# Kernel tuning notes

Hardware: AMD Instinct MI355X
Metric: run time of the kernel (lower is better)

The kernel has to match this reference:

```python
import jax, jax.numpy as jnp
import numpy as np

HEADS = 16
PHI = (1.0 + np.sqrt(5.0)) / 2.0


def setup_inputs() -> dict:
    key = jax.random.key(0)
    k1, k2, k3, k4 = jax.random.split(key, 4)
    B, L, D = 2, 2048, 1024
    x = jax.random.normal(k1, (B, L, D), dtype=jnp.float32)
    # nn.Linear(dim, 3*dim, bias=False): store as [D, 3D] for x @ W
    w_qkv = jax.random.normal(k2, (D, 3 * D), dtype=jnp.float32) * (D ** -0.5)
    w_proj = jax.random.normal(k3, (D, D), dtype=jnp.float32) * (D ** -0.5)
    b_proj = jax.random.normal(k4, (D,), dtype=jnp.float32) * 0.01
    return {"x": x, "w_qkv": w_qkv, "w_proj": w_proj, "b_proj": b_proj}


def phi_bias(L):
    # pos[i] = (i * phi) mod 1 ; bias = log(exp(-|pos_i - pos_j|) + 1e-8)
    pos = (jnp.arange(L, dtype=jnp.float32) * PHI) % 1.0
    dist = jnp.abs(pos[:, None] - pos[None, :])  # [L, L]
    return jnp.log(jnp.exp(-dist) + 1e-8)


def reference(x, w_qkv, w_proj, b_proj):
    B, L, D = x.shape
    H = HEADS
    Dh = D // H
    scale = Dh ** -0.5
    qkv = (x @ w_qkv).reshape(B, L, 3, H, Dh)
    q = jnp.transpose(qkv[:, :, 0], (0, 2, 1, 3))  # [B, H, L, Dh]
    k = jnp.transpose(qkv[:, :, 1], (0, 2, 1, 3))
    v = jnp.transpose(qkv[:, :, 2], (0, 2, 1, 3))
    attn = jnp.einsum("bhid,bhjd->bhij", q, k) * scale  # [B, H, L, L]
    attn = attn + phi_bias(L)[None, None]  # additive phi-distance bias
    attn = jax.nn.softmax(attn, axis=-1)
    out = jnp.einsum("bhij,bhjd->bhid", attn, v)  # [B, H, L, Dh]
    out = jnp.transpose(out, (0, 2, 1, 3)).reshape(B, L, D)
    return out @ w_proj + b_proj
```

## Files before the change

kernel.cpp:

```cpp
#include <hip/hip_runtime.h>
#include <math.h>


typedef _Float16 f16;
typedef _Float16 f16x4 __attribute__((ext_vector_type(4)));
typedef _Float16 f16x8 __attribute__((ext_vector_type(8)));
typedef float f32x4 __attribute__((ext_vector_type(4)));

#define MFMA32(a, b, c) __builtin_amdgcn_mfma_f32_16x16x32_f16(a, b, c, 0, 0, 0)

static constexpr int Bsz = 2, Lseq = 2048, Dm = 1024, H = 16, Dh = 64;
static constexpr int Mtot = Bsz * Lseq;
static constexpr int NQKV = 3 * Dm;
static constexpr float PHI_F = 1.61803398874989484820f;
static constexpr float LOG2E = 1.44269504088896f;
static constexpr float QS = 0.125f * LOG2E;
static constexpr float CSTEP = 0.55417527999932633f;

__device__ __forceinline__ void load16_to_lds(const f16* g, f16* l) {
  __builtin_amdgcn_global_load_lds(
      (const __attribute__((address_space(1))) unsigned int*)g,
      (__attribute__((address_space(3))) unsigned int*)l, 16, 0, 0);
}

__global__ __launch_bounds__(256) void prep_fused(
    const float* __restrict__ x, f16* __restrict__ xb,
    const float* __restrict__ wqkv, f16* __restrict__ wqkvT,
    const float* __restrict__ wproj, f16* __restrict__ wpT) {
  __shared__ float tile[32][33];
  int blk = blockIdx.x;
  if (blk < 4096) {
    int i = (blk * 256 + threadIdx.x) * 4;
    float4 v = *reinterpret_cast<const float4*>(x + i);
    f16 t[4] = {(f16)v.x, (f16)v.y, (f16)v.z, (f16)v.w};
    *reinterpret_cast<uint2*>(xb + i) = *reinterpret_cast<uint2*>(t);
    return;
  }
  const float* in;
  f16* out;
  int N, bx, by;
  if (blk < 7168) {
    int local = blk - 4096;
    bx = local % 96; by = local / 96; N = NQKV;
    in = wqkv; out = wqkvT;
  } else {
    int local = blk - 7168;
    bx = local & 31; by = local >> 5; N = Dm;
    in = wproj; out = wpT;
  }
  int n0 = bx * 32, k0 = by * 32;
  int tx = threadIdx.x & 31, ty = threadIdx.x >> 5;
#pragma unroll
  for (int r = 0; r < 32; r += 8)
    tile[ty + r][tx] = in[(size_t)(k0 + ty + r) * N + n0 + tx];
  __syncthreads();
#pragma unroll
  for (int r = 0; r < 32; r += 8)
    out[(size_t)(n0 + ty + r) * Dm + k0 + tx] = (f16)tile[tx][ty + r];
}

template <int MODE>
__global__ __launch_bounds__(256) void gemm_f16(
    const f16* __restrict__ A, const f16* __restrict__ Bt,
    int M, int N, int K,
    f16* __restrict__ qb, f16* __restrict__ kb, f16* __restrict__ vb,
    float* __restrict__ out, const float* __restrict__ bias) {
  constexpr int BM = (MODE == 0) ? 128 : 64;
  constexpr int MI = BM / 32;
  constexpr int AI = BM / 32;
  __shared__ f16 As[BM * 64];
  __shared__ f16 Bs[128 * 64];

  int tid = threadIdx.x;
  int wave = tid >> 6, lane = tid & 63;
  int quad = lane >> 4, l16 = lane & 15;
  int wm = (wave >> 1) * (MI * 16), wn = (wave & 1) * 64;

  int lid = blockIdx.x;
  int xcd = lid & 7, t = lid >> 3;
  int m0, n0;
  if (MODE == 0) {
    int mg = xcd >> 1, ng = xcd & 1;
    m0 = (mg * 8 + t / 12) * 128;
    n0 = (ng * 12 + t % 12) * 128;
  } else {
    m0 = (xcd * 8 + (t >> 3)) * 64;
    n0 = (t & 7) * 128;
  }

  const int gu = (lane & 7) ^ (lane >> 3);
  const f16* gA[AI];
  f16* lA[AI];
#pragma unroll
  for (int i = 0; i < AI; i++) {
    int it = wave * AI + i;
    gA[i] = A + (size_t)(m0 + it * 8 + (lane >> 3)) * K + gu * 8;
    lA[i] = As + it * 512;
  }
  const f16* gB[4];
  f16* lB[4];
#pragma unroll
  for (int i = 0; i < 4; i++) {
    int it = wave * 4 + i;
    gB[i] = Bt + (size_t)(n0 + it * 8 + (lane >> 3)) * K + gu * 8;
    lB[i] = Bs + it * 512;
  }

  f32x4 acc[MI][4] = {};

  for (int k0 = 0; k0 < K; k0 += 64) {
#pragma unroll
    for (int i = 0; i < AI; i++) load16_to_lds(gA[i] + k0, lA[i]);
#pragma unroll
    for (int i = 0; i < 4; i++) load16_to_lds(gB[i] + k0, lB[i]);
    __syncthreads();
#pragma unroll
    for (int s = 0; s < 2; s++) {
      f16x8 a[MI], b[4];
#pragma unroll
      for (int i = 0; i < MI; i++) {
        int row = wm + i * 16 + l16;
        a[i] = *reinterpret_cast<const f16x8*>(
            As + row * 64 + (((s * 4 + quad) ^ (l16 & 7)) * 8));
      }
#pragma unroll
      for (int j = 0; j < 4; j++) {
        int row = wn + j * 16 + l16;
        b[j] = *reinterpret_cast<const f16x8*>(
            Bs + row * 64 + (((s * 4 + quad) ^ (l16 & 7)) * 8));
      }
#pragma unroll
      for (int i = 0; i < MI; i++)
#pragma unroll
        for (int j = 0; j < 4; j++)
          acc[i][j] = MFMA32(a[i], b[j], acc[i][j]);
    }
    __syncthreads();
  }

#pragma unroll
  for (int i = 0; i < MI; i++) {
#pragma unroll
    for (int j = 0; j < 4; j++) {
      int n = n0 + wn + j * 16 + l16;
      if (MODE == 0) {
        int ty = n >> 10;
        int df = n & 1023;
        int h = df >> 6, dh = df & 63;
        int mb = m0 + wm + i * 16 + quad * 4;
        int b = mb >> 11, l = mb & 2047;
        int bhh = b * H + h;
        if (ty == 2) {
          int jj = l & 63;
          int jh = jj >> 5, rem = jj & 31;
          int qd = (rem & 15) >> 2;
          int e0 = (rem >= 16) ? 4 : 0;
          f16x4 tmp;
#pragma unroll
          for (int r = 0; r < 4; r++) tmp[r] = (f16)acc[i][j][r];
          *reinterpret_cast<uint2*>(
              vb + (size_t)bhh * (Dh * Lseq) + (l >> 6) * 4096 + dh * 64 +
              (jh * 4 + qd) * 8 + e0) = *reinterpret_cast<uint2*>(&tmp);
        } else {
          size_t idx = (((size_t)bhh) * Lseq + l) * Dh + dh;
          if (ty == 0) {
#pragma unroll
            for (int r = 0; r < 4; r++)
              qb[idx + (size_t)r * Dh] = (f16)(acc[i][j][r] * QS);
          } else {
#pragma unroll
            for (int r = 0; r < 4; r++)
              kb[idx + (size_t)r * Dh] = (f16)acc[i][j][r];
          }
        }
      } else {
#pragma unroll
        for (int r = 0; r < 4; r++) {
          int m = m0 + wm + i * 16 + quad * 4 + r;
          out[(size_t)m * N + n] = acc[i][j][r] + bias[n];
        }
      }
    }
  }
}

__global__ __launch_bounds__(512, 4) void attn_kernel(
    const f16* __restrict__ qb,
    const f16* __restrict__ kb,
    const f16* __restrict__ vb,
    f16* __restrict__ ctx) {
  __shared__ __align__(16) unsigned char smem[33280];
  f16* Ks = (f16*)smem;
  f16* Vs = (f16*)(smem + 8192);

  int id = blockIdx.x;
  int bh = (id & 7) * 4 + ((id >> 3) >> 4);
  int q0 = ((id >> 3) & 15) * 128;

  int tid = threadIdx.x, wave = tid >> 6, lane = tid & 63;
  int quad = lane >> 4, l16 = lane & 15;
  int jhalf = wave >> 2, qq = wave & 3;

  f16x8 qfrag[2][2];
  float pq[2];
#pragma unroll
  for (int set = 0; set < 2; set++) {
    int q = q0 + qq * 32 + set * 16 + l16;
    const f16* Qrow = qb + ((size_t)bh * Lseq + q) * Dh;
    qfrag[set][0] = *reinterpret_cast<const f16x8*>(Qrow + quad * 8);
    qfrag[set][1] = *reinterpret_cast<const f16x8*>(Qrow + 32 + quad * 8);
    pq[set] = fmodf((float)q * PHI_F, 1.0f);
  }

  float pk[2][4];
#pragma unroll
  for (int jb = 0; jb < 2; jb++)
#pragma unroll
    for (int r = 0; r < 4; r++) {
      int j = jhalf * 32 + jb * 16 + quad * 4 + r;
      pk[jb][r] = fmodf((float)j * PHI_F, 1.0f);
    }

  const f16* Kbh = kb + (size_t)bh * Lseq * Dh;
  const f16* Vbh = vb + (size_t)bh * Dh * Lseq;
  const int gu = (lane & 7) ^ (lane >> 3);
  int g8 = wave * 8 + (lane >> 3);
  const f16* gK = Kbh + (size_t)g8 * Dh + gu * 8;
  const f16* gV = Vbh + (size_t)g8 * 64 + gu * 8;
  f16* lK = Ks + wave * 512;
  f16* lV = Vs + wave * 512;

  const f16 one = (f16)1.0f;
  const f16x8 ones8 = {one, one, one, one, one, one, one, one};

  f32x4 acc_o[2][4] = {};
  f32x4 acc_l[2] = {};

  for (int j0 = 0; j0 < Lseq; j0 += 64) {
    __syncthreads();
    load16_to_lds(gK + (size_t)j0 * Dh, lK);
    load16_to_lds(gV + (size_t)j0 * 64, lV);
    __syncthreads();

    f32x4 accs[2][2] = {};
#pragma unroll
    for (int s = 0; s < 2; s++)
#pragma unroll
      for (int jb = 0; jb < 2; jb++) {
        f16x8 kf = *reinterpret_cast<const f16x8*>(
            Ks + (jhalf * 32 + jb * 16 + l16) * 64 + (((s * 4 + quad) ^ (l16 & 7)) * 8));
        accs[0][jb] = MFMA32(kf, qfrag[0][s], accs[0][jb]);
        accs[1][jb] = MFMA32(kf, qfrag[1][s], accs[1][jb]);
      }

    f16x8 pf8[2];
#pragma unroll
    for (int set = 0; set < 2; set++) {
#pragma unroll
      for (int jb = 0; jb < 2; jb++) {
        float p[4];
#pragma unroll
        for (int r = 0; r < 4; r++) {
          float d = pq[set] - pk[jb][r];
          float arg = fmaf(-LOG2E, fabsf(d), accs[set][jb][r]);
          p[r] = __builtin_amdgcn_exp2f(arg);
        }
        auto lo = __builtin_amdgcn_cvt_pkrtz(p[0], p[1]);
        auto hi = __builtin_amdgcn_cvt_pkrtz(p[2], p[3]);
        pf8[set][jb * 4 + 0] = lo[0];
        pf8[set][jb * 4 + 1] = lo[1];
        pf8[set][jb * 4 + 2] = hi[0];
        pf8[set][jb * 4 + 3] = hi[1];
      }
      acc_l[set] = MFMA32(ones8, pf8[set], acc_l[set]);
    }
#pragma unroll
    for (int jb = 0; jb < 2; jb++)
#pragma unroll
      for (int r = 0; r < 4; r++)
        pk[jb][r] = __builtin_amdgcn_fractf(pk[jb][r] + CSTEP);

#pragma unroll
    for (int dblk = 0; dblk < 4; dblk++) {
      int row = dblk * 16 + l16;
      f16x8 va = *reinterpret_cast<const f16x8*>(
          Vs + row * 64 + (((jhalf * 4 + quad) ^ (l16 & 7)) * 8));
      acc_o[0][dblk] = MFMA32(va, pf8[0], acc_o[0][dblk]);
      acc_o[1][dblk] = MFMA32(va, pf8[1], acc_o[1][dblk]);
    }
  }

  __syncthreads();
  float* Oex = (float*)smem;
  float* Lex = (float*)(smem + 32768);
  if (jhalf == 1) {
#pragma unroll
    for (int set = 0; set < 2; set++) {
#pragma unroll
      for (int dblk = 0; dblk < 4; dblk++)
#pragma unroll
        for (int r = 0; r < 4; r++)
          Oex[(((qq * 2 + set) * 4 + dblk) * 16 + quad * 4 + r) * 16 + l16] =
              acc_o[set][dblk][r];
      if (quad == 0) Lex[(qq * 2 + set) * 16 + l16] = acc_l[set][0];
    }
  }
  __syncthreads();
  if (jhalf == 0) {
    int b = bh >> 4, h = bh & 15;
#pragma unroll
    for (int set = 0; set < 2; set++) {
      float ltot = acc_l[set][0] + Lex[(qq * 2 + set) * 16 + l16];
      float inv = 1.0f / ltot;
      int q = q0 + qq * 32 + set * 16 + l16;
      f16* crow = ctx + (size_t)(b * Lseq + q) * Dm + h * 64;
#pragma unroll
      for (int dblk = 0; dblk < 4; dblk++) {
        f16x4 o;
#pragma unroll
        for (int r = 0; r < 4; r++) {
          float full = acc_o[set][dblk][r] +
              Oex[(((qq * 2 + set) * 4 + dblk) * 16 + quad * 4 + r) * 16 + l16];
          o[r] = (f16)(full * inv);
        }
        *reinterpret_cast<uint2*>(crow + dblk * 16 + quad * 4) =
            *reinterpret_cast<uint2*>(&o);
      }
    }
  }
}

extern "C" void kernel_launch(void* const* d_in, const int* in_sizes, int n_in,
                              void* d_out, int out_size, void* d_ws, size_t ws_size,
                              hipStream_t stream) {
  const float* x      = (const float*)d_in[0];
  const float* w_qkv  = (const float*)d_in[1];
  const float* w_proj = (const float*)d_in[2];
  const float* b_proj = (const float*)d_in[3];
  float* out = (float*)d_out;

  f16* xb    = (f16*)d_ws;
  f16* wqkvT = xb + (size_t)Mtot * Dm;
  f16* wpT   = wqkvT + (size_t)NQKV * Dm;
  f16* qb    = wpT + (size_t)Dm * Dm;
  f16* kb    = qb + (size_t)Bsz * H * Lseq * Dh;
  f16* vb    = kb + (size_t)Bsz * H * Lseq * Dh;
  f16* ctx   = vb + (size_t)Bsz * H * Lseq * Dh;

  prep_fused<<<8192, 256, 0, stream>>>(x, xb, w_qkv, wqkvT, w_proj, wpT);

  gemm_f16<0><<<768, 256, 0, stream>>>(
      xb, wqkvT, Mtot, NQKV, Dm, qb, kb, vb, nullptr, nullptr);

  attn_kernel<<<512, 512, 0, stream>>>(qb, kb, vb, ctx);

  gemm_f16<1><<<512, 256, 0, stream>>>(
      ctx, wpT, Mtot, Dm, Dm, nullptr, nullptr, nullptr, out, b_proj);
}
```

Measured before the change: 180.8 us.

## Double-buffer GEMM LDS tiles with prefetch and enlarge block tiles

```diff
diff --git a/kernel.cpp b/kernel.cpp
--- a/kernel.cpp
+++ b/kernel.cpp
@@ -60,83 +60,99 @@
 }
 
 template <int MODE>
-__global__ __launch_bounds__(256) void gemm_f16(
+__global__ __launch_bounds__(MODE == 0 ? 512 : 256, 2) void gemm_f16(
     const f16* __restrict__ A, const f16* __restrict__ Bt,
     int M, int N, int K,
     f16* __restrict__ qb, f16* __restrict__ kb, f16* __restrict__ vb,
     float* __restrict__ out, const float* __restrict__ bias) {
-  constexpr int BM = (MODE == 0) ? 128 : 64;
-  constexpr int MI = BM / 32;
-  constexpr int AI = BM / 32;
-  __shared__ f16 As[BM * 64];
-  __shared__ f16 Bs[128 * 64];
+  constexpr int BM = (MODE == 0) ? 256 : 128;
+  constexpr int BN = (MODE == 0) ? 256 : 128;
+  constexpr int NW = (MODE == 0) ? 8 : 4;
+  constexpr int MI = (MODE == 0) ? 8 : 4;
+  constexpr int WN = (MODE == 0) ? 4 : 2;
+  __shared__ f16 As[2 * BM * 64];
+  __shared__ f16 Bs[2 * BN * 64];
 
   int tid = threadIdx.x;
   int wave = tid >> 6, lane = tid & 63;
   int quad = lane >> 4, l16 = lane & 15;
-  int wm = (wave >> 1) * (MI * 16), wn = (wave & 1) * 64;
+  int warp_m = wave / WN, warp_n = wave % WN;
+  int wm = warp_m * (MI * 16), wn = warp_n * 64;
 
   int lid = blockIdx.x;
   int xcd = lid & 7, t = lid >> 3;
   int m0, n0;
   if (MODE == 0) {
     int mg = xcd >> 1, ng = xcd & 1;
-    m0 = (mg * 8 + t / 12) * 128;
-    n0 = (ng * 12 + t % 12) * 128;
+    m0 = (mg * 4 + t / 6) * 256;
+    n0 = (ng * 6 + t % 6) * 256;
   } else {
-    m0 = (xcd * 8 + (t >> 3)) * 64;
+    m0 = (xcd * 4 + (t >> 3)) * 128;
     n0 = (t & 7) * 128;
   }
 
   const int gu = (lane & 7) ^ (lane >> 3);
-  const f16* gA[AI];
-  f16* lA[AI];
-#pragma unroll
-  for (int i = 0; i < AI; i++) {
-    int it = wave * AI + i;
-    gA[i] = A + (size_t)(m0 + it * 8 + (lane >> 3)) * K + gu * 8;
-    lA[i] = As + it * 512;
-  }
+  const f16* gA[4];
   const f16* gB[4];
-  f16* lB[4];
 #pragma unroll
   for (int i = 0; i < 4; i++) {
-    int it = wave * 4 + i;
-    gB[i] = Bt + (size_t)(n0 + it * 8 + (lane >> 3)) * K + gu * 8;
-    lB[i] = Bs + it * 512;
-  }
+    int row = (i * NW + wave) * 8 + (lane >> 3);
+    gA[i] = A + (size_t)(m0 + row) * K + gu * 8;
+    gB[i] = Bt + (size_t)(n0 + row) * K + gu * 8;
+  }
+
+  auto stage = [&](int buf, int kn) __attribute__((always_inline)) {
+#pragma unroll
+    for (int i = 0; i < 4; i++)
+      load16_to_lds(gA[i] + kn, As + buf * (BM * 64) + (i * NW + wave) * 512);
+#pragma unroll
+    for (int i = 0; i < 4; i++)
+      load16_to_lds(gB[i] + kn, Bs + buf * (BN * 64) + (i * NW + wave) * 512);
+  };
 
   f32x4 acc[MI][4] = {};
 
-  for (int k0 = 0; k0 < K; k0 += 64) {
-#pragma unroll
-    for (int i = 0; i < AI; i++) load16_to_lds(gA[i] + k0, lA[i]);
-#pragma unroll
-    for (int i = 0; i < 4; i++) load16_to_lds(gB[i] + k0, lB[i]);
-    __syncthreads();
-#pragma unroll
-    for (int s = 0; s < 2; s++) {
-      f16x8 a[MI], b[4];
-#pragma unroll
-      for (int i = 0; i < MI; i++) {
-        int row = wm + i * 16 + l16;
-        a[i] = *reinterpret_cast<const f16x8*>(
-            As + row * 64 + (((s * 4 + quad) ^ (l16 & 7)) * 8));
-      }
-#pragma unroll
-      for (int j = 0; j < 4; j++) {
-        int row = wn + j * 16 + l16;
-        b[j] = *reinterpret_cast<const f16x8*>(
-            Bs + row * 64 + (((s * 4 + quad) ^ (l16 & 7)) * 8));
-      }
-#pragma unroll
-      for (int i = 0; i < MI; i++)
-#pragma unroll
-        for (int j = 0; j < 4; j++)
-          acc[i][j] = MFMA32(a[i], b[j], acc[i][j]);
-    }
-    __syncthreads();
-  }
+  stage(0, 0);
+  stage(1, 64);
+
+  int nt = K >> 6;
+#pragma unroll 1
+  for (int kt = 0; kt < nt; kt++) {
+    int buf = kt & 1;
+    asm volatile("s_waitcnt vmcnt(8)" ::: "memory");
+    __builtin_amdgcn_sched_barrier(0);
+    __builtin_amdgcn_s_barrier();
+    __builtin_amdgcn_sched_barrier(0);
+
+    const f16* Ab = As + buf * (BM * 64) + (wm + l16) * 64;
+    const f16* Bb = Bs + buf * (BN * 64) + (wn + l16) * 64;
+    f16x8 b[4][2];
+#pragma unroll
+    for (int nj = 0; nj < 4; nj++)
+#pragma unroll
+      for (int s = 0; s < 2; s++)
+        b[nj][s] = *reinterpret_cast<const f16x8*>(
+            Bb + nj * 16 * 64 + (((s * 4 + quad) ^ (l16 & 7)) * 8));
+#pragma unroll
+    for (int mi = 0; mi < MI; mi++) {
+      f16x8 a0 = *reinterpret_cast<const f16x8*>(
+          Ab + mi * 16 * 64 + ((quad ^ (l16 & 7)) * 8));
+      f16x8 a1 = *reinterpret_cast<const f16x8*>(
+          Ab + mi * 16 * 64 + (((4 + quad) ^ (l16 & 7)) * 8));
+#pragma unroll
+      for (int nj = 0; nj < 4; nj++) {
+        acc[mi][nj] = MFMA32(a0, b[nj][0], acc[mi][nj]);
+        acc[mi][nj] = MFMA32(a1, b[nj][1], acc[mi][nj]);
+      }
+    }
+
+    __builtin_amdgcn_sched_barrier(0);
+    __builtin_amdgcn_s_barrier();
+    __builtin_amdgcn_sched_barrier(0);
+    int kn = (kt + 2 < nt) ? (kt + 2) * 64 : 0;
+    stage(buf, kn);
+  }
+  asm volatile("s_waitcnt vmcnt(0)" ::: "memory");
 
 #pragma unroll
   for (int i = 0; i < MI; i++) {
@@ -349,11 +365,11 @@
 
   prep_fused<<<8192, 256, 0, stream>>>(x, xb, w_qkv, wqkvT, w_proj, wpT);
 
-  gemm_f16<0><<<768, 256, 0, stream>>>(
+  gemm_f16<0><<<192, 512, 0, stream>>>(
       xb, wqkvT, Mtot, NQKV, Dm, qb, kb, vb, nullptr, nullptr);
 
   attn_kernel<<<512, 512, 0, stream>>>(qb, kb, vb, ctx);
 
-  gemm_f16<1><<<512, 256, 0, stream>>>(
+  gemm_f16<1><<<256, 256, 0, stream>>>(
       ctx, wpT, Mtot, Dm, Dm, nullptr, nullptr, nullptr, out, b_proj);
 }
```

New measurement: 187.4 us. +3.6%, slower.

## Rewrite QKV GEMM as 256x256 tiles with double-buffered LDS pipelining

Applied to the files above, without the earlier changes.

```diff
diff --git a/kernel.cpp b/kernel.cpp
--- a/kernel.cpp
+++ b/kernel.cpp
@@ -21,6 +21,12 @@
   __builtin_amdgcn_global_load_lds(
       (const __attribute__((address_space(1))) unsigned int*)g,
       (__attribute__((address_space(3))) unsigned int*)l, 16, 0, 0);
+}
+
+__device__ __forceinline__ void barrier_fenced() {
+  __builtin_amdgcn_sched_barrier(0);
+  __builtin_amdgcn_s_barrier();
+  __builtin_amdgcn_sched_barrier(0);
 }
 
 __global__ __launch_bounds__(256) void prep_fused(
@@ -59,15 +65,194 @@
     out[(size_t)(n0 + ty + r) * Dm + k0 + tx] = (f16)tile[tx][ty + r];
 }
 
-template <int MODE>
-__global__ __launch_bounds__(256) void gemm_f16(
+__global__ __launch_bounds__(512, 2) void gemm_qkv(
     const f16* __restrict__ A, const f16* __restrict__ Bt,
-    int M, int N, int K,
-    f16* __restrict__ qb, f16* __restrict__ kb, f16* __restrict__ vb,
+    f16* __restrict__ qb, f16* __restrict__ kb, f16* __restrict__ vb) {
+  __shared__ f16 As[2 * 256 * 64];
+  __shared__ f16 Bs[2 * 256 * 64];
+
+  int tid = threadIdx.x;
+  int wave = tid >> 6, lane = tid & 63;
+  int quad = lane >> 4, l16 = lane & 15;
+  int warp_m = wave >> 2, warp_n = wave & 3;
+  int wm = warp_m * 128, wn = warp_n * 64;
+
+  int lid = blockIdx.x;
+  int xcd = lid & 7, t = lid >> 3;
+  int mg = xcd >> 1, ng = xcd & 1;
+  int m0 = (mg * 4 + t / 6) * 256;
+  int n0 = (ng * 6 + t % 6) * 256;
+
+  const int gu = (lane & 7) ^ (lane >> 3);
+  const f16* gAb = A + (size_t)(m0 + wave * 8 + (lane >> 3)) * Dm + gu * 8;
+  const f16* gBb = Bt + (size_t)(n0 + wave * 8 + (lane >> 3)) * Dm + gu * 8;
+
+  auto stageA = [&](int buf, int h, int kn) __attribute__((always_inline)) {
+#pragma unroll
+    for (int i = 0; i < 2; i++)
+      load16_to_lds(gAb + (size_t)(h * 128 + i * 64) * Dm + kn,
+                    As + buf * 16384 + (h * 128 + i * 64 + wave * 8) * 64);
+  };
+  auto stageB = [&](int buf, int h, int kn) __attribute__((always_inline)) {
+#pragma unroll
+    for (int i = 0; i < 2; i++)
+      load16_to_lds(gBb + (size_t)(h * 128 + i * 64) * Dm + kn,
+                    Bs + buf * 16384 + (h * 128 + i * 64 + wave * 8) * 64);
+  };
+
+  f32x4 acc[8][4] = {};
+
+  auto do_tile = [&](int buf, int t_) __attribute__((always_inline)) {
+    const f16* Ab = As + buf * 16384 + (wm + l16) * 64;
+    const f16* Bb = Bs + buf * 16384 + (wn + l16) * 64;
+    int nbuf = buf ^ 1;
+    int kA = ((t_ + 1) & 15) * 64;
+    int kB = ((t_ + 2) & 15) * 64;
+
+    f16x8 a[4][2], b0[2][2], b1[2][2];
+
+#pragma unroll
+    for (int m = 0; m < 4; m++)
+#pragma unroll
+      for (int s = 0; s < 2; s++)
+        a[m][s] = *reinterpret_cast<const f16x8*>(
+            Ab + m * 16 * 64 + (((s * 4 + quad) ^ (l16 & 7)) * 8));
+#pragma unroll
+    for (int n = 0; n < 2; n++)
+#pragma unroll
+      for (int s = 0; s < 2; s++)
+        b0[n][s] = *reinterpret_cast<const f16x8*>(
+            Bb + n * 16 * 64 + (((s * 4 + quad) ^ (l16 & 7)) * 8));
+    stageA(nbuf, 0, kA);
+    barrier_fenced();
+    asm volatile("s_waitcnt lgkmcnt(0)" ::: "memory");
+    __builtin_amdgcn_sched_barrier(0);
+    __builtin_amdgcn_s_setprio(1);
+#pragma unroll
+    for (int m = 0; m < 4; m++)
+#pragma unroll
+      for (int n = 0; n < 2; n++) {
+        acc[m][n] = MFMA32(a[m][0], b0[n][0], acc[m][n]);
+        acc[m][n] = MFMA32(a[m][1], b0[n][1], acc[m][n]);
+      }
+    __builtin_amdgcn_s_setprio(0);
+    barrier_fenced();
+
+#pragma unroll
+    for (int n = 0; n < 2; n++)
+#pragma unroll
+      for (int s = 0; s < 2; s++)
+        b1[n][s] = *reinterpret_cast<const f16x8*>(
+            Bb + (2 + n) * 16 * 64 + (((s * 4 + quad) ^ (l16 & 7)) * 8));
+    stageA(nbuf, 1, kA);
+    barrier_fenced();
+    asm volatile("s_waitcnt lgkmcnt(0)" ::: "memory");
+    __builtin_amdgcn_sched_barrier(0);
+    __builtin_amdgcn_s_setprio(1);
+#pragma unroll
+    for (int m = 0; m < 4; m++)
+#pragma unroll
+      for (int n = 0; n < 2; n++) {
+        acc[m][2 + n] = MFMA32(a[m][0], b1[n][0], acc[m][2 + n]);
+        acc[m][2 + n] = MFMA32(a[m][1], b1[n][1], acc[m][2 + n]);
+      }
+    __builtin_amdgcn_s_setprio(0);
+    barrier_fenced();
+
+#pragma unroll
+    for (int m = 0; m < 4; m++)
+#pragma unroll
+      for (int s = 0; s < 2; s++)
+        a[m][s] = *reinterpret_cast<const f16x8*>(
+            Ab + (4 + m) * 16 * 64 + (((s * 4 + quad) ^ (l16 & 7)) * 8));
+    stageB(buf, 0, kB);
+    barrier_fenced();
+    asm volatile("s_waitcnt lgkmcnt(0)" ::: "memory");
+    __builtin_amdgcn_sched_barrier(0);
+    __builtin_amdgcn_s_setprio(1);
+#pragma unroll
+    for (int m = 0; m < 4; m++)
+#pragma unroll
+      for (int n = 0; n < 2; n++) {
+        acc[4 + m][n] = MFMA32(a[m][0], b0[n][0], acc[4 + m][n]);
+        acc[4 + m][n] = MFMA32(a[m][1], b0[n][1], acc[4 + m][n]);
+      }
+    __builtin_amdgcn_s_setprio(0);
+    barrier_fenced();
+
+    stageB(buf, 1, kB);
+    asm volatile("s_waitcnt vmcnt(4)" ::: "memory");
+    barrier_fenced();
+    __builtin_amdgcn_s_setprio(1);
+#pragma unroll
+    for (int m = 0; m < 4; m++)
+#pragma unroll
+      for (int n = 0; n < 2; n++) {
+        acc[4 + m][2 + n] = MFMA32(a[m][0], b1[n][0], acc[4 + m][2 + n]);
+        acc[4 + m][2 + n] = MFMA32(a[m][1], b1[n][1], acc[4 + m][2 + n]);
+      }
+    __builtin_amdgcn_s_setprio(0);
+    barrier_fenced();
+  };
+
+  stageA(0, 0, 0);
+  stageA(0, 1, 0);
+  stageB(0, 0, 0);
+  stageB(0, 1, 0);
+  stageB(1, 0, 64);
+  stageB(1, 1, 64);
+  asm volatile("s_waitcnt vmcnt(4)" ::: "memory");
+  barrier_fenced();
+
+#pragma unroll 1
+  for (int tt = 0; tt < 16; tt += 2) {
+    do_tile(0, tt);
+    do_tile(1, tt + 1);
+  }
+  asm volatile("s_waitcnt vmcnt(0)" ::: "memory");
+
+#pragma unroll
+  for (int i = 0; i < 8; i++) {
+#pragma unroll
+    for (int j = 0; j < 4; j++) {
+      int n = n0 + wn + j * 16 + l16;
+      int ty = n >> 10;
+      int df = n & 1023;
+      int h = df >> 6, dh = df & 63;
+      int mb = m0 + wm + i * 16 + quad * 4;
+      int b = mb >> 11, l = mb & 2047;
+      int bhh = b * H + h;
+      if (ty == 2) {
+        int jj = l & 63;
+        int jh = jj >> 5, rem = jj & 31;
+        int qd = (rem & 15) >> 2;
+        int e0 = (rem >= 16) ? 4 : 0;
+        f16x4 tmp;
+#pragma unroll
+        for (int r = 0; r < 4; r++) tmp[r] = (f16)acc[i][j][r];
+        *reinterpret_cast<uint2*>(
+            vb + (size_t)bhh * (Dh * Lseq) + (l >> 6) * 4096 + dh * 64 +
+            (jh * 4 + qd) * 8 + e0) = *reinterpret_cast<uint2*>(&tmp);
+      } else {
+        size_t idx = (((size_t)bhh) * Lseq + l) * Dh + dh;
+        if (ty == 0) {
+#pragma unroll
+          for (int r = 0; r < 4; r++)
+            qb[idx + (size_t)r * Dh] = (f16)(acc[i][j][r] * QS);
+        } else {
+#pragma unroll
+          for (int r = 0; r < 4; r++)
+            kb[idx + (size_t)r * Dh] = (f16)acc[i][j][r];
+        }
+      }
+    }
+  }
+}
+
+__global__ __launch_bounds__(256) void gemm_proj(
+    const f16* __restrict__ A, const f16* __restrict__ Bt,
     float* __restrict__ out, const float* __restrict__ bias) {
-  constexpr int BM = (MODE == 0) ? 128 : 64;
-  constexpr int MI = BM / 32;
-  constexpr int AI = BM / 32;
+  constexpr int BM = 64, MI = 2, AI = 2;
   __shared__ f16 As[BM * 64];
   __shared__ f16 Bs[128 * 64];
 
@@ -78,15 +263,8 @@
 
   int lid = blockIdx.x;
   int xcd = lid & 7, t = lid >> 3;
-  int m0, n0;
-  if (MODE == 0) {
-    int mg = xcd >> 1, ng = xcd & 1;
-    m0 = (mg * 8 + t / 12) * 128;
-    n0 = (ng * 12 + t % 12) * 128;
-  } else {
-    m0 = (xcd * 8 + (t >> 3)) * 64;
-    n0 = (t & 7) * 128;
-  }
+  int m0 = (xcd * 8 + (t >> 3)) * 64;
+  int n0 = (t & 7) * 128;
 
   const int gu = (lane & 7) ^ (lane >> 3);
   const f16* gA[AI];
@@ -94,7 +272,7 @@
 #pragma unroll
   for (int i = 0; i < AI; i++) {
     int it = wave * AI + i;
-    gA[i] = A + (size_t)(m0 + it * 8 + (lane >> 3)) * K + gu * 8;
+    gA[i] = A + (size_t)(m0 + it * 8 + (lane >> 3)) * Dm + gu * 8;
     lA[i] = As + it * 512;
   }
   const f16* gB[4];
@@ -102,13 +280,13 @@
 #pragma unroll
   for (int i = 0; i < 4; i++) {
     int it = wave * 4 + i;
-    gB[i] = Bt + (size_t)(n0 + it * 8 + (lane >> 3)) * K + gu * 8;
+    gB[i] = Bt + (size_t)(n0 + it * 8 + (lane >> 3)) * Dm + gu * 8;
     lB[i] = Bs + it * 512;
   }
 
   f32x4 acc[MI][4] = {};
 
-  for (int k0 = 0; k0 < K; k0 += 64) {
+  for (int k0 = 0; k0 < Dm; k0 += 64) {
 #pragma unroll
     for (int i = 0; i < AI; i++) load16_to_lds(gA[i] + k0, lA[i]);
 #pragma unroll
@@ -139,49 +317,16 @@
   }
 
 #pragma unroll
-  for (int i = 0; i < MI; i++) {
+  for (int i = 0; i < MI; i++)
 #pragma unroll
     for (int j = 0; j < 4; j++) {
       int n = n0 + wn + j * 16 + l16;
-      if (MODE == 0) {
-        int ty = n >> 10;
-        int df = n & 1023;
-        int h = df >> 6, dh = df & 63;
-        int mb = m0 + wm + i * 16 + quad * 4;
-        int b = mb >> 11, l = mb & 2047;
-        int bhh = b * H + h;
-        if (ty == 2) {
-          int jj = l & 63;
-          int jh = jj >> 5, rem = jj & 31;
-          int qd = (rem & 15) >> 2;
-          int e0 = (rem >= 16) ? 4 : 0;
-          f16x4 tmp;
-#pragma unroll
-          for (int r = 0; r < 4; r++) tmp[r] = (f16)acc[i][j][r];
-          *reinterpret_cast<uint2*>(
-              vb + (size_t)bhh * (Dh * Lseq) + (l >> 6) * 4096 + dh * 64 +
-              (jh * 4 + qd) * 8 + e0) = *reinterpret_cast<uint2*>(&tmp);
-        } else {
-          size_t idx = (((size_t)bhh) * Lseq + l) * Dh + dh;
-          if (ty == 0) {
-#pragma unroll
-            for (int r = 0; r < 4; r++)
-              qb[idx + (size_t)r * Dh] = (f16)(acc[i][j][r] * QS);
-          } else {
-#pragma unroll
-            for (int r = 0; r < 4; r++)
-              kb[idx + (size_t)r * Dh] = (f16)acc[i][j][r];
-          }
-        }
-      } else {
-#pragma unroll
-        for (int r = 0; r < 4; r++) {
-          int m = m0 + wm + i * 16 + quad * 4 + r;
-          out[(size_t)m * N + n] = acc[i][j][r] + bias[n];
-        }
-      }
-    }
-  }
+#pragma unroll
+      for (int r = 0; r < 4; r++) {
+        int m = m0 + wm + i * 16 + quad * 4 + r;
+        out[(size_t)m * Dm + n] = acc[i][j][r] + bias[n];
+      }
+    }
 }
 
 __global__ __launch_bounds__(512, 4) void attn_kernel(
@@ -349,11 +494,9 @@
 
   prep_fused<<<8192, 256, 0, stream>>>(x, xb, w_qkv, wqkvT, w_proj, wpT);
 
-  gemm_f16<0><<<768, 256, 0, stream>>>(
-      xb, wqkvT, Mtot, NQKV, Dm, qb, kb, vb, nullptr, nullptr);
+  gemm_qkv<<<192, 512, 0, stream>>>(xb, wqkvT, qb, kb, vb);
 
   attn_kernel<<<512, 512, 0, stream>>>(qb, kb, vb, ctx);
 
-  gemm_f16<1><<<512, 256, 0, stream>>>(
-      ctx, wpT, Mtot, Dm, Dm, nullptr, nullptr, nullptr, out, b_proj);
-}
+  gemm_proj<<<512, 256, 0, stream>>>(ctx, wpT, out, b_proj);
+}
```

New measurement: 179.9 us. About the same (-0.5%).
